# Kernel tuning notes

Measured on AMD Instinct MI355X. Metric: run time of the kernel, lower is better.

The kernel has to match this reference:

```python
import jax, jax.numpy as jnp
import numpy as np

S = 4096
T_STEPS = 2048

def setup_inputs() -> dict:
    key = jax.random.key(0)
    k1, k2, k3 = jax.random.split(key, 3)
    # initial log-prior over S states
    log_M0 = jax.nn.log_softmax(jax.random.normal(k1, (S,), dtype=jnp.float32))
    # transition log-probs: log_trans[i, j] = log p(x_t = i | x_{t-1} = j)
    # (logsumexp in the torch code is over dim=1 = previous state, so columns normalize)
    log_trans = jax.nn.log_softmax(jax.random.normal(k2, (S, S), dtype=jnp.float32), axis=0)
    # per-step emission log-likelihoods log f_t(y_t | x_t), t = 0..T
    log_emit = 0.5 * jax.random.normal(k3, (T_STEPS + 1, S), dtype=jnp.float32)
    return {"log_M0": log_M0, "log_trans": log_trans, "log_emit": log_emit, "T": T_STEPS}

def reference(log_M0, log_trans, log_emit, T):
    # initialise(): unnormalized filter at t=0
    unnorm0 = log_M0 + log_emit[0]                       # [S]
    lf0 = jax.nn.logsumexp(unnorm0)                      # scalar log-normalizer
    filt0 = unnorm0 - lf0

    def step(carry, emit_t):
        filt, lik = carry
        # prediction_i = logsumexp_j( filter_j + log_trans[i, j] )
        pred = jax.nn.logsumexp(filt[None, :] + log_trans, axis=1)   # [S]
        unnorm = pred + emit_t                                        # [S]
        lf = jax.nn.logsumexp(unnorm)
        return (unnorm - lf, lik + lf), None

    (_, likelihood), _ = jax.lax.scan(step, (filt0, lf0), log_emit[1:T + 1])
    # forward() returns the accumulated sum of per-step likelihood factors = total log-likelihood
    return likelihood
```

## Files before the change

kernel.cpp:

```cpp
#include <hip/hip_runtime.h>
#include <hip/hip_bf16.h>

#define SS 4096
#define TT 2048

typedef float v4f __attribute__((ext_vector_type(4)));


__device__ __forceinline__ void llc_load4x4(const v4f* p,
                                            v4f& a, v4f& b, v4f& c, v4f& d) {
  asm volatile(
      "global_load_dwordx4 %0, %4, off sc0 sc1\n\t"
      "global_load_dwordx4 %1, %5, off sc0 sc1\n\t"
      "global_load_dwordx4 %2, %6, off sc0 sc1\n\t"
      "global_load_dwordx4 %3, %7, off sc0 sc1\n\t"
      "s_waitcnt vmcnt(0)"
      : "=&v"(a), "=&v"(b), "=&v"(c), "=&v"(d)
      : "v"(p), "v"(p + 256), "v"(p + 512), "v"(p + 768)
      : "memory");
}

__device__ __forceinline__ void llc_store4_drain(v4f* p, v4f v) {
  asm volatile("global_store_dwordx4 %0, %1, off sc0 sc1\n\t"
               "s_waitcnt vmcnt(0)"
               :: "v"(p), "v"(v) : "memory");
}


__device__ __forceinline__ unsigned short f2bf_rn(float f) {
  unsigned int u = __float_as_uint(f);
  u += 0x7FFFu + ((u >> 16) & 1u);
  return (unsigned short)(u >> 16);
}

__device__ __forceinline__ unsigned orsgn(v4f v, unsigned e) {
  return (__float_as_uint(v.x) ^ e) | (__float_as_uint(v.y) ^ e)
       | (__float_as_uint(v.z) ^ e) | (__float_as_uint(v.w) ^ e);
}

__device__ __forceinline__ uint4 xorsgn(v4f v, unsigned e) {
  uint4 r;
  r.x = __float_as_uint(v.x) ^ e;  r.y = __float_as_uint(v.y) ^ e;
  r.z = __float_as_uint(v.z) ^ e;  r.w = __float_as_uint(v.w) ^ e;
  return r;
}

__device__ __forceinline__ float dot8(uint4 u, v4f qa, v4f qb, float acc) {
  acc = fmaf(__uint_as_float(u.x << 16),          qa.x, acc);
  acc = fmaf(__uint_as_float(u.x & 0xFFFF0000u),  qa.y, acc);
  acc = fmaf(__uint_as_float(u.y << 16),          qa.z, acc);
  acc = fmaf(__uint_as_float(u.y & 0xFFFF0000u),  qa.w, acc);
  acc = fmaf(__uint_as_float(u.z << 16),          qb.x, acc);
  acc = fmaf(__uint_as_float(u.z & 0xFFFF0000u),  qb.y, acc);
  acc = fmaf(__uint_as_float(u.w << 16),          qb.z, acc);
  acc = fmaf(__uint_as_float(u.w & 0xFFFF0000u),  qb.w, acc);
  return acc;
}

__global__ void prep_E(const float* __restrict__ lt, unsigned short* __restrict__ E) {
  size_t base = ((size_t)blockIdx.x * 256 + threadIdx.x) * 8;
  float4 a = ((const float4*)(lt + base))[0];
  float4 b = ((const float4*)(lt + base))[1];
  uint4 o;
  o.x = (unsigned)f2bf_rn(__expf(a.x)) | ((unsigned)f2bf_rn(__expf(a.y)) << 16);
  o.y = (unsigned)f2bf_rn(__expf(a.z)) | ((unsigned)f2bf_rn(__expf(a.w)) << 16);
  o.z = (unsigned)f2bf_rn(__expf(b.x)) | ((unsigned)f2bf_rn(__expf(b.y)) << 16);
  o.w = (unsigned)f2bf_rn(__expf(b.z)) | ((unsigned)f2bf_rn(__expf(b.w)) << 16);
  ((uint4*)(E + base))[0] = o;
}

__global__ void init_q(const float* __restrict__ m0, const float* __restrict__ emit,
                       float* __restrict__ q) {
  int i = blockIdx.x * 256 + threadIdx.x;
  q[i] = __expf(m0[i] + emit[i]);
}

__global__ void __launch_bounds__(256, 1)
hmm_fwd(const unsigned short* __restrict__ E, const float* __restrict__ emit,
        float* q, float* out) {
  __shared__ unsigned short es[16 * SS];
  __shared__ float qs[SS];
  __shared__ float wsum[4];
  const int b    = blockIdx.x;
  const int tid  = threadIdx.x;
  const int wave = tid >> 6;
  const int lane = tid & 63;
  const int row0 = (b << 4) + (wave << 2);

  {
    const uint4* src = (const uint4*)(E + ((size_t)b << 4) * SS);
    uint4* dst = (uint4*)es;
#pragma unroll
    for (int i = 0; i < 32; ++i)
      dst[tid + (i << 8)] = src[tid + (i << 8)];
  }
  __syncthreads();

  const uint4* ev = (const uint4*)es;
  const uint4* e0 = ev + (size_t)((wave << 2) + 0) * 512;
  const uint4* e1 = ev + (size_t)((wave << 2) + 1) * 512;
  const uint4* e2 = ev + (size_t)((wave << 2) + 2) * 512;
  const uint4* e3 = ev + (size_t)((wave << 2) + 3) * 512;

  for (int t = 1; t <= TT; ++t) {
    const unsigned e = (unsigned)(((t - 1) >> 1) & 1) << 31;
    {
      const v4f* qsrc4 = (const v4f*)(q + ((t - 1) & 1) * SS);
      v4f va, vb, vc, vd;
      for (;;) {
        llc_load4x4(qsrc4 + tid, va, vb, vc, vd);
        unsigned o = orsgn(va, e) | orsgn(vb, e) | orsgn(vc, e) | orsgn(vd, e);
        if (!(o >> 31)) break;
      }
      uint4* qs4 = (uint4*)qs;
      qs4[tid]       = xorsgn(va, e);
      qs4[tid + 256] = xorsgn(vb, e);
      qs4[tid + 512] = xorsgn(vc, e);
      qs4[tid + 768] = xorsgn(vd, e);
    }
    __syncthreads();

    v4f em;
    if (lane == 0) em = *(const v4f*)(emit + (size_t)t * SS + row0);

    float acc0 = 0.f, acc1 = 0.f, acc2 = 0.f, acc3 = 0.f;
#pragma unroll
    for (int k = 0; k < 8; ++k) {
      int vi = (k << 6) + lane;
      const v4f* qp = (const v4f*)(qs + (k << 9) + (lane << 3));
      v4f qa = qp[0], qb = qp[1];
      acc0 = dot8(e0[vi], qa, qb, acc0);
      acc1 = dot8(e1[vi], qa, qb, acc1);
      acc2 = dot8(e2[vi], qa, qb, acc2);
      acc3 = dot8(e3[vi], qa, qb, acc3);
    }
#pragma unroll
    for (int m = 32; m > 0; m >>= 1) {
      acc0 += __shfl_xor(acc0, m);
      acc1 += __shfl_xor(acc1, m);
      acc2 += __shfl_xor(acc2, m);
      acc3 += __shfl_xor(acc3, m);
    }

    float* qdst = q + (t & 1) * SS;
    if (lane == 0) {
      float scale = ((t & 255) == 0) ? 0x1p-46f : 1.0f;
      if ((t >> 1) & 1) scale = -scale;
      v4f r;
      r.x = acc0 * (__expf(em.x) * scale);
      r.y = acc1 * (__expf(em.y) * scale);
      r.z = acc2 * (__expf(em.z) * scale);
      r.w = acc3 * (__expf(em.w) * scale);
      llc_store4_drain((v4f*)(qdst + row0), r);
    }
    __syncthreads();
  }

  if (b == 0) {
    const v4f* qf4 = (const v4f*)q;
    v4f va, vb, vc, vd;
    for (;;) {
      llc_load4x4(qf4 + tid, va, vb, vc, vd);
      unsigned o = orsgn(va, 0) | orsgn(vb, 0) | orsgn(vc, 0) | orsgn(vd, 0);
      if (!(o >> 31)) break;
    }
    float s = va.x + va.y + va.z + va.w + vb.x + vb.y + vb.z + vb.w
            + vc.x + vc.y + vc.z + vc.w + vd.x + vd.y + vd.z + vd.w;
#pragma unroll
    for (int m = 32; m > 0; m >>= 1) s += __shfl_xor(s, m);
    if (lane == 0) wsum[wave] = s;
    __syncthreads();
    if (tid == 0) {
      float tot = wsum[0] + wsum[1] + wsum[2] + wsum[3];
      out[0] = logf(tot) + 368.0f * 0.693147180559945f;
    }
  }
}

extern "C" void kernel_launch(void* const* d_in, const int* in_sizes, int n_in,
                              void* d_out, int out_size, void* d_ws, size_t ws_size,
                              hipStream_t stream) {
  const float* log_M0    = (const float*)d_in[0];
  const float* log_trans = (const float*)d_in[1];
  const float* log_emit  = (const float*)d_in[2];

  unsigned short* E = (unsigned short*)d_ws;
  float* q  = (float*)((char*)d_ws + (size_t)SS * SS * 2);
  float* out = (float*)d_out;

  hipLaunchKernelGGL(prep_E, dim3((SS * SS) / 2048), dim3(256), 0, stream, log_trans, E);
  hipLaunchKernelGGL(init_q, dim3(SS / 256), dim3(256), 0, stream, log_M0, log_emit, q);
  hipLaunchKernelGGL(hmm_fwd, dim3(256), dim3(256), 0, stream, E, log_emit, q, out);
}
```

Before: 4.977 ms.

## Use 512 threads per block and split the K dimension across waves

```diff
diff --git a/kernel.cpp b/kernel.cpp
--- a/kernel.cpp
+++ b/kernel.cpp
@@ -3,25 +3,23 @@
 
 #define SS 4096
 #define TT 2048
+#define RP 4104
 
 typedef float v4f __attribute__((ext_vector_type(4)));
 
 
-__device__ __forceinline__ void llc_load4x4(const v4f* p,
-                                            v4f& a, v4f& b, v4f& c, v4f& d) {
+__device__ __forceinline__ void llc_load4x2(const v4f* p, v4f& a, v4f& b) {
   asm volatile(
-      "global_load_dwordx4 %0, %4, off sc0 sc1\n\t"
-      "global_load_dwordx4 %1, %5, off sc0 sc1\n\t"
-      "global_load_dwordx4 %2, %6, off sc0 sc1\n\t"
-      "global_load_dwordx4 %3, %7, off sc0 sc1\n\t"
+      "global_load_dwordx4 %0, %2, off sc0 sc1\n\t"
+      "global_load_dwordx4 %1, %3, off sc0 sc1\n\t"
       "s_waitcnt vmcnt(0)"
-      : "=&v"(a), "=&v"(b), "=&v"(c), "=&v"(d)
-      : "v"(p), "v"(p + 256), "v"(p + 512), "v"(p + 768)
+      : "=&v"(a), "=&v"(b)
+      : "v"(p), "v"(p + 512)
       : "memory");
 }
 
-__device__ __forceinline__ void llc_store4_drain(v4f* p, v4f v) {
-  asm volatile("global_store_dwordx4 %0, %1, off sc0 sc1\n\t"
+__device__ __forceinline__ void llc_store_drain(float* p, float v) {
+  asm volatile("global_store_dword %0, %1, off sc0 sc1\n\t"
                "s_waitcnt vmcnt(0)"
                :: "v"(p), "v"(v) : "memory");
 }
@@ -75,103 +73,89 @@
   q[i] = __expf(m0[i] + emit[i]);
 }
 
-__global__ void __launch_bounds__(256, 1)
+__global__ void __launch_bounds__(512, 1)
 hmm_fwd(const unsigned short* __restrict__ E, const float* __restrict__ emit,
         float* q, float* out) {
-  __shared__ unsigned short es[16 * SS];
+  __shared__ unsigned short es[16 * RP];
   __shared__ float qs[SS];
-  __shared__ float wsum[4];
+  __shared__ float part[8 * 16];
+  __shared__ float wsum[8];
   const int b    = blockIdx.x;
   const int tid  = threadIdx.x;
-  const int wave = tid >> 6;
+  const int w    = tid >> 6;
   const int lane = tid & 63;
-  const int row0 = (b << 4) + (wave << 2);
+  const int r    = lane & 15;
+  const int g    = lane >> 4;
 
   {
     const uint4* src = (const uint4*)(E + ((size_t)b << 4) * SS);
-    uint4* dst = (uint4*)es;
 #pragma unroll
-    for (int i = 0; i < 32; ++i)
-      dst[tid + (i << 8)] = src[tid + (i << 8)];
+    for (int i = 0; i < 16; ++i) {
+      int idx = tid + (i << 9);
+      int row = idx >> 9;
+      int gr  = idx & 511;
+      ((uint4*)(es + row * RP))[gr] = src[(row << 9) + gr];
+    }
   }
   __syncthreads();
 
-  const uint4* ev = (const uint4*)es;
-  const uint4* e0 = ev + (size_t)((wave << 2) + 0) * 512;
-  const uint4* e1 = ev + (size_t)((wave << 2) + 1) * 512;
-  const uint4* e2 = ev + (size_t)((wave << 2) + 2) * 512;
-  const uint4* e3 = ev + (size_t)((wave << 2) + 3) * 512;
+  const uint4* ep  = (const uint4*)(es + r * RP + (w << 9) + (g << 7));
+  const v4f*   qp0 = (const v4f*)(qs + (w << 9) + (g << 7));
 
   for (int t = 1; t <= TT; ++t) {
     const unsigned e = (unsigned)(((t - 1) >> 1) & 1) << 31;
     {
       const v4f* qsrc4 = (const v4f*)(q + ((t - 1) & 1) * SS);
-      v4f va, vb, vc, vd;
+      v4f va, vb;
       for (;;) {
-        llc_load4x4(qsrc4 + tid, va, vb, vc, vd);
-        unsigned o = orsgn(va, e) | orsgn(vb, e) | orsgn(vc, e) | orsgn(vd, e);
+        llc_load4x2(qsrc4 + tid, va, vb);
+        unsigned o = orsgn(va, e) | orsgn(vb, e);
         if (!(o >> 31)) break;
       }
       uint4* qs4 = (uint4*)qs;
       qs4[tid]       = xorsgn(va, e);
-      qs4[tid + 256] = xorsgn(vb, e);
-      qs4[tid + 512] = xorsgn(vc, e);
-      qs4[tid + 768] = xorsgn(vd, e);
+      qs4[tid + 512] = xorsgn(vb, e);
     }
     __syncthreads();
 
-    v4f em;
-    if (lane == 0) em = *(const v4f*)(emit + (size_t)t * SS + row0);
+    float em = 0.f;
+    if (tid < 16) em = emit[(size_t)t * SS + (b << 4) + tid];
 
-    float acc0 = 0.f, acc1 = 0.f, acc2 = 0.f, acc3 = 0.f;
+    float acc = 0.f;
 #pragma unroll
-    for (int k = 0; k < 8; ++k) {
-      int vi = (k << 6) + lane;
-      const v4f* qp = (const v4f*)(qs + (k << 9) + (lane << 3));
-      v4f qa = qp[0], qb = qp[1];
-      acc0 = dot8(e0[vi], qa, qb, acc0);
-      acc1 = dot8(e1[vi], qa, qb, acc1);
-      acc2 = dot8(e2[vi], qa, qb, acc2);
-      acc3 = dot8(e3[vi], qa, qb, acc3);
-    }
-#pragma unroll
-    for (int m = 32; m > 0; m >>= 1) {
-      acc0 += __shfl_xor(acc0, m);
-      acc1 += __shfl_xor(acc1, m);
-      acc2 += __shfl_xor(acc2, m);
-      acc3 += __shfl_xor(acc3, m);
-    }
+    for (int j = 0; j < 16; ++j)
+      acc = dot8(ep[j], qp0[2 * j], qp0[2 * j + 1], acc);
 
-    float* qdst = q + (t & 1) * SS;
-    if (lane == 0) {
+    acc += __shfl_xor(acc, 16);
+    acc += __shfl_xor(acc, 32);
+    if (lane < 16) part[(w << 4) + lane] = acc;
+    __syncthreads();
+
+    if (tid < 16) {
+      float s = part[tid]      + part[tid + 16] + part[tid + 32] + part[tid + 48]
+              + part[tid + 64] + part[tid + 80] + part[tid + 96] + part[tid + 112];
       float scale = ((t & 255) == 0) ? 0x1p-46f : 1.0f;
       if ((t >> 1) & 1) scale = -scale;
-      v4f r;
-      r.x = acc0 * (__expf(em.x) * scale);
-      r.y = acc1 * (__expf(em.y) * scale);
-      r.z = acc2 * (__expf(em.z) * scale);
-      r.w = acc3 * (__expf(em.w) * scale);
-      llc_store4_drain((v4f*)(qdst + row0), r);
+      llc_store_drain(q + (t & 1) * SS + (b << 4) + tid, s * (__expf(em) * scale));
     }
-    __syncthreads();
   }
 
   if (b == 0) {
     const v4f* qf4 = (const v4f*)q;
-    v4f va, vb, vc, vd;
+    v4f va, vb;
     for (;;) {
-      llc_load4x4(qf4 + tid, va, vb, vc, vd);
-      unsigned o = orsgn(va, 0) | orsgn(vb, 0) | orsgn(vc, 0) | orsgn(vd, 0);
+      llc_load4x2(qf4 + tid, va, vb);
+      unsigned o = orsgn(va, 0) | orsgn(vb, 0);
       if (!(o >> 31)) break;
     }
-    float s = va.x + va.y + va.z + va.w + vb.x + vb.y + vb.z + vb.w
-            + vc.x + vc.y + vc.z + vc.w + vd.x + vd.y + vd.z + vd.w;
+    float s = va.x + va.y + va.z + va.w + vb.x + vb.y + vb.z + vb.w;
 #pragma unroll
     for (int m = 32; m > 0; m >>= 1) s += __shfl_xor(s, m);
-    if (lane == 0) wsum[wave] = s;
+    if (lane == 0) wsum[w] = s;
     __syncthreads();
     if (tid == 0) {
-      float tot = wsum[0] + wsum[1] + wsum[2] + wsum[3];
+      float tot = wsum[0] + wsum[1] + wsum[2] + wsum[3]
+                + wsum[4] + wsum[5] + wsum[6] + wsum[7];
       out[0] = logf(tot) + 368.0f * 0.693147180559945f;
     }
   }
@@ -190,5 +174,5 @@
 
   hipLaunchKernelGGL(prep_E, dim3((SS * SS) / 2048), dim3(256), 0, stream, log_trans, E);
   hipLaunchKernelGGL(init_q, dim3(SS / 256), dim3(256), 0, stream, log_M0, log_emit, q);
-  hipLaunchKernelGGL(hmm_fwd, dim3(256), dim3(256), 0, stream, E, log_emit, q, out);
+  hipLaunchKernelGGL(hmm_fwd, dim3(256), dim3(512), 0, stream, E, log_emit, q, out);
 }
```

After: 7.132 ms. 1.43x slower.

## Hold fp32 transition rows in registers instead of bf16 in shared memory

Applied to the files above, without the earlier changes.

```diff
diff --git a/kernel.cpp b/kernel.cpp
--- a/kernel.cpp
+++ b/kernel.cpp
@@ -20,18 +20,12 @@
       : "memory");
 }
 
-__device__ __forceinline__ void llc_store4_drain(v4f* p, v4f v) {
-  asm volatile("global_store_dwordx4 %0, %1, off sc0 sc1\n\t"
+__device__ __forceinline__ void llc_store_drain(float* p, float v) {
+  asm volatile("global_store_dword %0, %1, off sc0 sc1\n\t"
                "s_waitcnt vmcnt(0)"
                :: "v"(p), "v"(v) : "memory");
 }
 
-
-__device__ __forceinline__ unsigned short f2bf_rn(float f) {
-  unsigned int u = __float_as_uint(f);
-  u += 0x7FFFu + ((u >> 16) & 1u);
-  return (unsigned short)(u >> 16);
-}
 
 __device__ __forceinline__ unsigned orsgn(v4f v, unsigned e) {
   return (__float_as_uint(v.x) ^ e) | (__float_as_uint(v.y) ^ e)
@@ -45,30 +39,6 @@
   return r;
 }
 
-__device__ __forceinline__ float dot8(uint4 u, v4f qa, v4f qb, float acc) {
-  acc = fmaf(__uint_as_float(u.x << 16),          qa.x, acc);
-  acc = fmaf(__uint_as_float(u.x & 0xFFFF0000u),  qa.y, acc);
-  acc = fmaf(__uint_as_float(u.y << 16),          qa.z, acc);
-  acc = fmaf(__uint_as_float(u.y & 0xFFFF0000u),  qa.w, acc);
-  acc = fmaf(__uint_as_float(u.z << 16),          qb.x, acc);
-  acc = fmaf(__uint_as_float(u.z & 0xFFFF0000u),  qb.y, acc);
-  acc = fmaf(__uint_as_float(u.w << 16),          qb.z, acc);
-  acc = fmaf(__uint_as_float(u.w & 0xFFFF0000u),  qb.w, acc);
-  return acc;
-}
-
-__global__ void prep_E(const float* __restrict__ lt, unsigned short* __restrict__ E) {
-  size_t base = ((size_t)blockIdx.x * 256 + threadIdx.x) * 8;
-  float4 a = ((const float4*)(lt + base))[0];
-  float4 b = ((const float4*)(lt + base))[1];
-  uint4 o;
-  o.x = (unsigned)f2bf_rn(__expf(a.x)) | ((unsigned)f2bf_rn(__expf(a.y)) << 16);
-  o.y = (unsigned)f2bf_rn(__expf(a.z)) | ((unsigned)f2bf_rn(__expf(a.w)) << 16);
-  o.z = (unsigned)f2bf_rn(__expf(b.x)) | ((unsigned)f2bf_rn(__expf(b.y)) << 16);
-  o.w = (unsigned)f2bf_rn(__expf(b.z)) | ((unsigned)f2bf_rn(__expf(b.w)) << 16);
-  ((uint4*)(E + base))[0] = o;
-}
-
 __global__ void init_q(const float* __restrict__ m0, const float* __restrict__ emit,
                        float* __restrict__ q) {
   int i = blockIdx.x * 256 + threadIdx.x;
@@ -76,31 +46,37 @@
 }
 
 __global__ void __launch_bounds__(256, 1)
-hmm_fwd(const unsigned short* __restrict__ E, const float* __restrict__ emit,
+hmm_fwd(const float* __restrict__ lt, const float* __restrict__ emit,
         float* q, float* out) {
-  __shared__ unsigned short es[16 * SS];
-  __shared__ float qs[SS];
+  __shared__ float qs[4224];
   __shared__ float wsum[4];
   const int b    = blockIdx.x;
   const int tid  = threadIdx.x;
-  const int wave = tid >> 6;
+  const int w    = tid >> 6;
   const int lane = tid & 63;
-  const int row0 = (b << 4) + (wave << 2);
+  const int r    = lane & 3;
+  const int s    = lane >> 2;
+  const int grow = (b << 4) + (w << 2) + r;
 
+  float eR[256];
   {
-    const uint4* src = (const uint4*)(E + ((size_t)b << 4) * SS);
-    uint4* dst = (uint4*)es;
+    const float* rowp = lt + (size_t)grow * SS;
 #pragma unroll
-    for (int i = 0; i < 32; ++i)
-      dst[tid + (i << 8)] = src[tid + (i << 8)];
+    for (int st = 0; st < 2; ++st)
+#pragma unroll
+      for (int k = 0; k < 32; ++k) {
+        v4f v = *(const v4f*)(rowp + 128 * (s + 16 * st) + 4 * k);
+        int j = (st * 32 + k) * 4;
+        eR[j + 0] = __expf(v.x);
+        eR[j + 1] = __expf(v.y);
+        eR[j + 2] = __expf(v.z);
+        eR[j + 3] = __expf(v.w);
+      }
   }
-  __syncthreads();
 
-  const uint4* ev = (const uint4*)es;
-  const uint4* e0 = ev + (size_t)((wave << 2) + 0) * 512;
-  const uint4* e1 = ev + (size_t)((wave << 2) + 1) * 512;
-  const uint4* e2 = ev + (size_t)((wave << 2) + 2) * 512;
-  const uint4* e3 = ev + (size_t)((wave << 2) + 3) * 512;
+  const int pbase = tid + (tid >> 5);
+  const v4f* qA = (const v4f*)qs + 33 * s;
+  const v4f* qB = qA + 33 * 16;
 
   for (int t = 1; t <= TT; ++t) {
     const unsigned e = (unsigned)(((t - 1) >> 1) & 1) << 31;
@@ -113,45 +89,39 @@
         if (!(o >> 31)) break;
       }
       uint4* qs4 = (uint4*)qs;
-      qs4[tid]       = xorsgn(va, e);
-      qs4[tid + 256] = xorsgn(vb, e);
-      qs4[tid + 512] = xorsgn(vc, e);
-      qs4[tid + 768] = xorsgn(vd, e);
+      qs4[pbase]       = xorsgn(va, e);
+      qs4[pbase + 264] = xorsgn(vb, e);
+      qs4[pbase + 528] = xorsgn(vc, e);
+      qs4[pbase + 792] = xorsgn(vd, e);
     }
     __syncthreads();
 
-    v4f em;
-    if (lane == 0) em = *(const v4f*)(emit + (size_t)t * SS + row0);
+    float em = emit[(size_t)t * SS + grow];
 
-    float acc0 = 0.f, acc1 = 0.f, acc2 = 0.f, acc3 = 0.f;
+    float a0 = 0.f, a1 = 0.f, a2 = 0.f, a3 = 0.f;
 #pragma unroll
-    for (int k = 0; k < 8; ++k) {
-      int vi = (k << 6) + lane;
-      const v4f* qp = (const v4f*)(qs + (k << 9) + (lane << 3));
-      v4f qa = qp[0], qb = qp[1];
-      acc0 = dot8(e0[vi], qa, qb, acc0);
-      acc1 = dot8(e1[vi], qa, qb, acc1);
-      acc2 = dot8(e2[vi], qa, qb, acc2);
-      acc3 = dot8(e3[vi], qa, qb, acc3);
+    for (int k = 0; k < 32; ++k) {
+      v4f qa = qA[k], qb = qB[k];
+      a0 = fmaf(eR[4 * k + 0], qa.x, a0);
+      a1 = fmaf(eR[4 * k + 1], qa.y, a1);
+      a2 = fmaf(eR[4 * k + 2], qa.z, a2);
+      a3 = fmaf(eR[4 * k + 3], qa.w, a3);
+      a0 = fmaf(eR[128 + 4 * k + 0], qb.x, a0);
+      a1 = fmaf(eR[128 + 4 * k + 1], qb.y, a1);
+      a2 = fmaf(eR[128 + 4 * k + 2], qb.z, a2);
+      a3 = fmaf(eR[128 + 4 * k + 3], qb.w, a3);
     }
-#pragma unroll
-    for (int m = 32; m > 0; m >>= 1) {
-      acc0 += __shfl_xor(acc0, m);
-      acc1 += __shfl_xor(acc1, m);
-      acc2 += __shfl_xor(acc2, m);
-      acc3 += __shfl_xor(acc3, m);
-    }
+    float acc = (a0 + a1) + (a2 + a3);
 
-    float* qdst = q + (t & 1) * SS;
-    if (lane == 0) {
+    acc += __shfl_xor(acc, 4);
+    acc += __shfl_xor(acc, 8);
+    acc += __shfl_xor(acc, 16);
+    acc += __shfl_xor(acc, 32);
+
+    if (lane < 4) {
       float scale = ((t & 255) == 0) ? 0x1p-46f : 1.0f;
       if ((t >> 1) & 1) scale = -scale;
-      v4f r;
-      r.x = acc0 * (__expf(em.x) * scale);
-      r.y = acc1 * (__expf(em.y) * scale);
-      r.z = acc2 * (__expf(em.z) * scale);
-      r.w = acc3 * (__expf(em.w) * scale);
-      llc_store4_drain((v4f*)(qdst + row0), r);
+      llc_store_drain(q + (t & 1) * SS + grow, acc * (__expf(em) * scale));
     }
     __syncthreads();
   }
@@ -164,11 +134,11 @@
       unsigned o = orsgn(va, 0) | orsgn(vb, 0) | orsgn(vc, 0) | orsgn(vd, 0);
       if (!(o >> 31)) break;
     }
-    float s = va.x + va.y + va.z + va.w + vb.x + vb.y + vb.z + vb.w
-            + vc.x + vc.y + vc.z + vc.w + vd.x + vd.y + vd.z + vd.w;
+    float sm = va.x + va.y + va.z + va.w + vb.x + vb.y + vb.z + vb.w
+             + vc.x + vc.y + vc.z + vc.w + vd.x + vd.y + vd.z + vd.w;
 #pragma unroll
-    for (int m = 32; m > 0; m >>= 1) s += __shfl_xor(s, m);
-    if (lane == 0) wsum[wave] = s;
+    for (int m = 32; m > 0; m >>= 1) sm += __shfl_xor(sm, m);
+    if (lane == 0) wsum[w] = sm;
     __syncthreads();
     if (tid == 0) {
       float tot = wsum[0] + wsum[1] + wsum[2] + wsum[3];
@@ -184,11 +154,9 @@
   const float* log_trans = (const float*)d_in[1];
   const float* log_emit  = (const float*)d_in[2];
 
-  unsigned short* E = (unsigned short*)d_ws;
-  float* q  = (float*)((char*)d_ws + (size_t)SS * SS * 2);
+  float* q   = (float*)d_ws;
   float* out = (float*)d_out;
 
-  hipLaunchKernelGGL(prep_E, dim3((SS * SS) / 2048), dim3(256), 0, stream, log_trans, E);
   hipLaunchKernelGGL(init_q, dim3(SS / 256), dim3(256), 0, stream, log_M0, log_emit, q);
-  hipLaunchKernelGGL(hmm_fwd, dim3(256), dim3(256), 0, stream, E, log_emit, q, out);
+  hipLaunchKernelGGL(hmm_fwd, dim3(256), dim3(256), 0, stream, log_trans, log_emit, q, out);
 }
```

After: 6.381 ms. +28.2%, slower.

## Pipeline spin-poll loads, pad LDS q staging, prefetch emissions, drop trailing barrier

Applied to the files above, without the earlier changes.

```diff
diff --git a/kernel.cpp b/kernel.cpp
--- a/kernel.cpp
+++ b/kernel.cpp
@@ -7,17 +7,28 @@
 typedef float v4f __attribute__((ext_vector_type(4)));
 
 
-__device__ __forceinline__ void llc_load4x4(const v4f* p,
-                                            v4f& a, v4f& b, v4f& c, v4f& d) {
+__device__ __forceinline__ void llc_issue4(const v4f* p,
+                                           v4f& a, v4f& b, v4f& c, v4f& d) {
   asm volatile(
       "global_load_dwordx4 %0, %4, off sc0 sc1\n\t"
       "global_load_dwordx4 %1, %5, off sc0 sc1\n\t"
       "global_load_dwordx4 %2, %6, off sc0 sc1\n\t"
-      "global_load_dwordx4 %3, %7, off sc0 sc1\n\t"
-      "s_waitcnt vmcnt(0)"
+      "global_load_dwordx4 %3, %7, off sc0 sc1"
       : "=&v"(a), "=&v"(b), "=&v"(c), "=&v"(d)
       : "v"(p), "v"(p + 256), "v"(p + 512), "v"(p + 768)
       : "memory");
+}
+
+__device__ __forceinline__ void llc_wait4(v4f& a, v4f& b, v4f& c, v4f& d) {
+  asm volatile("s_waitcnt vmcnt(4)"
+               : "+v"(a), "+v"(b), "+v"(c), "+v"(d) :: "memory");
+}
+
+__device__ __forceinline__ void llc_drain8(v4f& a0, v4f& a1, v4f& a2, v4f& a3,
+                                           v4f& b0, v4f& b1, v4f& b2, v4f& b3) {
+  asm volatile("s_waitcnt vmcnt(0)"
+               : "+v"(a0), "+v"(a1), "+v"(a2), "+v"(a3),
+                 "+v"(b0), "+v"(b1), "+v"(b2), "+v"(b3) :: "memory");
 }
 
 __device__ __forceinline__ void llc_store4_drain(v4f* p, v4f v) {
@@ -57,6 +68,16 @@
   return acc;
 }
 
+__device__ __forceinline__ void stage_q(float* qs, int tid, unsigned e,
+                                        v4f va, v4f vb, v4f vc, v4f vd) {
+  uint4* qs4 = (uint4*)qs;
+  int p0 = tid + (tid >> 1);
+  qs4[p0]        = xorsgn(va, e);
+  qs4[p0 + 384]  = xorsgn(vb, e);
+  qs4[p0 + 768]  = xorsgn(vc, e);
+  qs4[p0 + 1152] = xorsgn(vd, e);
+}
+
 __global__ void prep_E(const float* __restrict__ lt, unsigned short* __restrict__ E) {
   size_t base = ((size_t)blockIdx.x * 256 + threadIdx.x) * 8;
   float4 a = ((const float4*)(lt + base))[0];
@@ -79,13 +100,13 @@
 hmm_fwd(const unsigned short* __restrict__ E, const float* __restrict__ emit,
         float* q, float* out) {
   __shared__ unsigned short es[16 * SS];
-  __shared__ float qs[SS];
+  __shared__ float qs[6144];
   __shared__ float wsum[4];
   const int b    = blockIdx.x;
   const int tid  = threadIdx.x;
-  const int wave = tid >> 6;
+  const int w    = tid >> 6;
   const int lane = tid & 63;
-  const int row0 = (b << 4) + (wave << 2);
+  const int row0 = (b << 4) + (w << 2);
 
   {
     const uint4* src = (const uint4*)(E + ((size_t)b << 4) * SS);
@@ -97,38 +118,44 @@
   __syncthreads();
 
   const uint4* ev = (const uint4*)es;
-  const uint4* e0 = ev + (size_t)((wave << 2) + 0) * 512;
-  const uint4* e1 = ev + (size_t)((wave << 2) + 1) * 512;
-  const uint4* e2 = ev + (size_t)((wave << 2) + 2) * 512;
-  const uint4* e3 = ev + (size_t)((wave << 2) + 3) * 512;
+  const uint4* e0 = ev + (size_t)((w << 2) + 0) * 512;
+  const uint4* e1 = ev + (size_t)((w << 2) + 1) * 512;
+  const uint4* e2 = ev + (size_t)((w << 2) + 2) * 512;
+  const uint4* e3 = ev + (size_t)((w << 2) + 3) * 512;
+
+  v4f em = {0.f, 0.f, 0.f, 0.f};
+  if (lane == 0) em = *(const v4f*)(emit + (size_t)1 * SS + row0);
 
   for (int t = 1; t <= TT; ++t) {
     const unsigned e = (unsigned)(((t - 1) >> 1) & 1) << 31;
     {
-      const v4f* qsrc4 = (const v4f*)(q + ((t - 1) & 1) * SS);
-      v4f va, vb, vc, vd;
+      const v4f* p = (const v4f*)(q + ((t - 1) & 1) * SS) + tid;
+      v4f a0, a1, a2, a3, b0, b1, b2, b3;
+      llc_issue4(p, a0, a1, a2, a3);
       for (;;) {
-        llc_load4x4(qsrc4 + tid, va, vb, vc, vd);
-        unsigned o = orsgn(va, e) | orsgn(vb, e) | orsgn(vc, e) | orsgn(vd, e);
-        if (!(o >> 31)) break;
+        llc_issue4(p, b0, b1, b2, b3);
+        llc_wait4(a0, a1, a2, a3);
+        if (!((orsgn(a0, e) | orsgn(a1, e) | orsgn(a2, e) | orsgn(a3, e)) >> 31)) {
+          stage_q(qs, tid, e, a0, a1, a2, a3);
+          break;
+        }
+        llc_issue4(p, a0, a1, a2, a3);
+        llc_wait4(b0, b1, b2, b3);
+        if (!((orsgn(b0, e) | orsgn(b1, e) | orsgn(b2, e) | orsgn(b3, e)) >> 31)) {
+          stage_q(qs, tid, e, b0, b1, b2, b3);
+          break;
+        }
       }
-      uint4* qs4 = (uint4*)qs;
-      qs4[tid]       = xorsgn(va, e);
-      qs4[tid + 256] = xorsgn(vb, e);
-      qs4[tid + 512] = xorsgn(vc, e);
-      qs4[tid + 768] = xorsgn(vd, e);
+      llc_drain8(a0, a1, a2, a3, b0, b1, b2, b3);
     }
     __syncthreads();
-
-    v4f em;
-    if (lane == 0) em = *(const v4f*)(emit + (size_t)t * SS + row0);
 
     float acc0 = 0.f, acc1 = 0.f, acc2 = 0.f, acc3 = 0.f;
 #pragma unroll
     for (int k = 0; k < 8; ++k) {
       int vi = (k << 6) + lane;
-      const v4f* qp = (const v4f*)(qs + (k << 9) + (lane << 3));
-      v4f qa = qp[0], qb = qp[1];
+      const v4f* qpair = (const v4f*)(qs + 768 * k + 12 * lane);
+      v4f qa = qpair[0], qb = qpair[1];
       acc0 = dot8(e0[vi], qa, qb, acc0);
       acc1 = dot8(e1[vi], qa, qb, acc1);
       acc2 = dot8(e2[vi], qa, qb, acc2);
@@ -152,23 +179,26 @@
       r.z = acc2 * (__expf(em.z) * scale);
       r.w = acc3 * (__expf(em.w) * scale);
       llc_store4_drain((v4f*)(qdst + row0), r);
-    }
-    __syncthreads();
+      int tn = (t < TT) ? t + 1 : t;
+      em = *(const v4f*)(emit + (size_t)tn * SS + row0);
+    }
   }
 
   if (b == 0) {
-    const v4f* qf4 = (const v4f*)q;
+    const v4f* qf4 = (const v4f*)q + tid;
     v4f va, vb, vc, vd;
     for (;;) {
-      llc_load4x4(qf4 + tid, va, vb, vc, vd);
-      unsigned o = orsgn(va, 0) | orsgn(vb, 0) | orsgn(vc, 0) | orsgn(vd, 0);
-      if (!(o >> 31)) break;
+      llc_issue4(qf4, va, vb, vc, vd);
+      asm volatile("s_waitcnt vmcnt(0)"
+                   : "+v"(va), "+v"(vb), "+v"(vc), "+v"(vd) :: "memory");
+      if (!((orsgn(va, 0) | orsgn(vb, 0) | orsgn(vc, 0) | orsgn(vd, 0)) >> 31))
+        break;
     }
     float s = va.x + va.y + va.z + va.w + vb.x + vb.y + vb.z + vb.w
             + vc.x + vc.y + vc.z + vc.w + vd.x + vd.y + vd.z + vd.w;
 #pragma unroll
     for (int m = 32; m > 0; m >>= 1) s += __shfl_xor(s, m);
-    if (lane == 0) wsum[wave] = s;
+    if (lane == 0) wsum[w] = s;
     __syncthreads();
     if (tid == 0) {
       float tot = wsum[0] + wsum[1] + wsum[2] + wsum[3];
```

New measurement: 5.695 ms. 1.14x slower.
